# Kernel optimization log

Hardware: AMD Instinct MI355X
Metric: run time of the kernel (lower is better)

Reference implementation:

```python
import jax, jax.numpy as jnp
import numpy as np

GAMMA = 1.0
INPUT_DIM = 512
NUM_CENTERS = 4096
BATCH = 16384


def setup_inputs() -> dict:
    key = jax.random.key(0)
    kx, kc = jax.random.split(key)
    x = jax.random.normal(kx, (BATCH, INPUT_DIM), dtype=jnp.float32)
    centers = jax.random.normal(kc, (NUM_CENTERS, INPUT_DIM), dtype=jnp.float32)
    return {"x": x, "centers": centers}


def reference(x, centers):
    x_sq = jnp.sum(x * x, axis=-1, keepdims=True)            # [B, 1]
    c_sq = jnp.sum(centers * centers, axis=-1)               # [C]
    cross = jnp.einsum("bd,cd->bc", x, centers)              # [B, C]
    dist_sq = x_sq - 2.0 * cross + c_sq[None, :]
    return jnp.exp(-GAMMA * dist_sq)
```

## Files before the change

### kernel.cpp

```cpp
#include <hip/hip_runtime.h>
#include <stdint.h>

#define M_DIM 16384
#define N_DIM 4096
#define K_DIM 512

typedef int v8i __attribute__((ext_vector_type(8)));
typedef float f32x16 __attribute__((ext_vector_type(16)));
typedef float f32x4v __attribute__((ext_vector_type(4)));

typedef __attribute__((address_space(3))) uint32_t lds_u32_t;
typedef const __attribute__((address_space(1))) uint32_t glob_u32_t;

__device__ __forceinline__ void gload16(const void* g, void* l) {
    __builtin_amdgcn_global_load_lds((glob_u32_t*)g, (lds_u32_t*)l, 16, 0, 0);
}

__global__ __launch_bounds__(256)
void convert_norm_kernel(const float* __restrict__ X, const float* __restrict__ C,
                         uint8_t* __restrict__ Apack, uint8_t* __restrict__ Bf8,
                         float* __restrict__ xsq, float* __restrict__ csq) {
    const int wave = threadIdx.x >> 6;
    const int lane = threadIdx.x & 63;
    const int row = blockIdx.x * 4 + wave;

    const float* src;
    uint8_t* dst;
    float* nrm;
    int r;
    size_t off;
    if (row < M_DIM) {
        src = X; dst = Apack; nrm = xsq; r = row;
        off = (size_t)((r >> 5) * 8 + (lane >> 3)) * 2048
            + ((lane >> 2) & 1) * 1024 + (r & 31) * 32 + (lane & 3) * 8;
    } else {
        src = C; dst = Bf8; nrm = csq; r = row - M_DIM;
        off = (size_t)r * K_DIM + lane * 8;
    }

    const float4* p = (const float4*)(src + (size_t)r * K_DIM) + lane * 2;
    float4 a = p[0], b = p[1];
    uint32_t lo = 0, hi = 0;
    lo = __builtin_amdgcn_cvt_pk_fp8_f32(a.x, a.y, lo, false);
    lo = __builtin_amdgcn_cvt_pk_fp8_f32(a.z, a.w, lo, true);
    hi = __builtin_amdgcn_cvt_pk_fp8_f32(b.x, b.y, hi, false);
    hi = __builtin_amdgcn_cvt_pk_fp8_f32(b.z, b.w, hi, true);
    *(uint2*)(dst + off) = make_uint2(lo, hi);

    float s = a.x*a.x + a.y*a.y + a.z*a.z + a.w*a.w
            + b.x*b.x + b.y*b.y + b.z*b.z + b.w*b.w;
    #pragma unroll
    for (int o2 = 32; o2 > 0; o2 >>= 1) s += __shfl_down(s, o2, 64);
    if (lane == 0) nrm[r] = s;
}

__global__ __launch_bounds__(256, 4)
void rbf_mfma_kernel(const uint8_t* __restrict__ Apack, const uint8_t* __restrict__ B8,
                     const float* __restrict__ xsq, const float* __restrict__ csq,
                     float* __restrict__ out) {
    __shared__ uint8_t Bs[128 * 128];

    const int tid = threadIdx.x;
    const int lv  = tid & 63;
    const int w   = tid >> 6;
    const int h   = lv >> 5;
    const int r31 = lv & 31;

    const int bn = (blockIdx.x & 31) * 128;
    const int bm = (blockIdx.x >> 5) * 128;

    const int tr = tid >> 3;
    const int tc = tid & 7;
    const int cc = (tc - tr) & 7;
    const uint8_t* gB = B8 + (size_t)(bn + 4 * tr) * K_DIM + cc * 16;
    uint8_t* BsW = Bs + w * 1024;

    const uint8_t* aB = Apack + (size_t)((bm >> 5) + w) * 16384 + h * 1024 + r31 * 32;

    const uint8_t* bRow = Bs + r31 * 128;

    f32x16 acc[4] = {};

    for (int kk = 0; kk < 4; ++kk) {
        const int koff = kk * 128;
        #pragma unroll
        for (int R = 0; R < 4; ++R)
            gload16(gB + koff + (size_t)R * K_DIM, BsW + R * 4096);

        uint4 a0[2], a1[2];
        #pragma unroll
        for (int ksl = 0; ksl < 2; ++ksl) {
            const uint8_t* ap = aB + (2 * kk + ksl) * 2048;
            a0[ksl] = *(const uint4*)(ap);
            a1[ksl] = *(const uint4*)(ap + 16);
        }
        __syncthreads();

        #pragma unroll
        for (int ksl = 0; ksl < 2; ++ksl) {
            v8i av = (v8i){(int)a0[ksl].x, (int)a0[ksl].y, (int)a0[ksl].z, (int)a0[ksl].w,
                           (int)a1[ksl].x, (int)a1[ksl].y, (int)a1[ksl].z, (int)a1[ksl].w};
            const int c0 = ksl * 4 + 2 * h;
            const int s0 = ((c0 + 0 + r31) & 7) * 16;
            const int s1 = ((c0 + 1 + r31) & 7) * 16;
            #pragma unroll
            for (int j = 0; j < 4; ++j) {
                uint4 lo = *(const uint4*)(bRow + j * 4096 + s0);
                uint4 hi = *(const uint4*)(bRow + j * 4096 + s1);
                v8i bv = (v8i){(int)lo.x, (int)lo.y, (int)lo.z, (int)lo.w,
                               (int)hi.x, (int)hi.y, (int)hi.z, (int)hi.w};
                acc[j] = __builtin_amdgcn_mfma_scale_f32_32x32x64_f8f6f4(
                    av, bv, acc[j],
                    0 , 0 ,
                    0, 0x7F7F7F7Fu, 0, 0x7F7F7F7Fu);
            }
        }
        if (kk < 3) __syncthreads();
    }

    const float4 cs4 = *(const float4*)(csq + bn + 4 * r31);
    const int mbase = bm + 32 * w + 4 * h;

    #pragma unroll
    for (int g = 0; g < 4; ++g) {
        const float4 xs4 = *(const float4*)(xsq + mbase + 8 * g);
        #pragma unroll
        for (int rr = 0; rr < 4; ++rr) {
            const int reg = g * 4 + rr;
            const float xs = (rr == 0) ? xs4.x : (rr == 1) ? xs4.y
                           : (rr == 2) ? xs4.z : xs4.w;
            const int gm = mbase + 8 * g + rr;
            f32x4v o;
            o.x = __expf(-(xs - 2.0f * acc[0][reg] + cs4.x));
            o.y = __expf(-(xs - 2.0f * acc[1][reg] + cs4.y));
            o.z = __expf(-(xs - 2.0f * acc[2][reg] + cs4.z));
            o.w = __expf(-(xs - 2.0f * acc[3][reg] + cs4.w));
            __builtin_nontemporal_store(
                o, (f32x4v*)(out + (size_t)gm * N_DIM + bn + 4 * r31));
        }
    }
}

extern "C" void kernel_launch(void* const* d_in, const int* in_sizes, int n_in,
                              void* d_out, int out_size, void* d_ws, size_t ws_size,
                              hipStream_t stream) {
    const float* X = (const float*)d_in[0];
    const float* C = (const float*)d_in[1];
    float* out = (float*)d_out;

    uint8_t* Apack = (uint8_t*)d_ws;
    uint8_t* Bf8 = Apack + (size_t)M_DIM * K_DIM;
    float* xsq = (float*)(Bf8 + (size_t)N_DIM * K_DIM);
    float* csq = xsq + M_DIM;

    convert_norm_kernel<<<(M_DIM + N_DIM) / 4, 256, 0, stream>>>(X, C, Apack, Bf8, xsq, csq);
    rbf_mfma_kernel<<<(M_DIM / 128) * (N_DIM / 128), 256, 0, stream>>>(Apack, Bf8, xsq, csq, out);
}
```

Before: 301.1 us.

## Double K-chunk size for B tile and software-pipeline A fragment loads

Enlarges the shared B tile from 128 to 256 K-bytes per stage, so the K loop runs 2 iterations instead of 4 and needs half as many block barriers. The LDS swizzle changes to a 16-slot rotation, and the global-to-LDS copy mapping is rewritten to match. A fragments are now prefetched one K-slice ahead inside the inner loop rather than all loaded before the barrier. The cost is 32 KB of LDS per block instead of 16 KB, which may reduce occupancy.

```diff
diff --git a/kernel.cpp b/kernel.cpp
--- a/kernel.cpp
+++ b/kernel.cpp
@@ -58,7 +58,7 @@
 void rbf_mfma_kernel(const uint8_t* __restrict__ Apack, const uint8_t* __restrict__ B8,
                      const float* __restrict__ xsq, const float* __restrict__ csq,
                      float* __restrict__ out) {
-    __shared__ uint8_t Bs[128 * 128];
+    __shared__ uint8_t Bs[128 * 256];
 
     const int tid = threadIdx.x;
     const int lv  = tid & 63;
@@ -69,44 +69,46 @@
     const int bn = (blockIdx.x & 31) * 128;
     const int bm = (blockIdx.x >> 5) * 128;
 
-    const int tr = tid >> 3;
-    const int tc = tid & 7;
-    const int cc = (tc - tr) & 7;
-    const uint8_t* gB = B8 + (size_t)(bn + 4 * tr) * K_DIM + cc * 16;
+    const int q  = 4 * w + (lv >> 4);
+    const int s  = lv & 15;
+    const int cb = (s - q) & 15;
+    const uint8_t* gB0 = B8 + (size_t)(bn + 4 * q) * K_DIM + cb * 16;
     uint8_t* BsW = Bs + w * 1024;
 
     const uint8_t* aB = Apack + (size_t)((bm >> 5) + w) * 16384 + h * 1024 + r31 * 32;
 
-    const uint8_t* bRow = Bs + r31 * 128;
+    const uint8_t* bRow = Bs + r31 * 256;
 
     f32x16 acc[4] = {};
 
-    for (int kk = 0; kk < 4; ++kk) {
-        const int koff = kk * 128;
+    #pragma unroll
+    for (int kk = 0; kk < 2; ++kk) {
         #pragma unroll
-        for (int R = 0; R < 4; ++R)
-            gload16(gB + koff + (size_t)R * K_DIM, BsW + R * 4096);
-
-        uint4 a0[2], a1[2];
-        #pragma unroll
-        for (int ksl = 0; ksl < 2; ++ksl) {
-            const uint8_t* ap = aB + (2 * kk + ksl) * 2048;
-            a0[ksl] = *(const uint4*)(ap);
-            a1[ksl] = *(const uint4*)(ap + 16);
+        for (int R = 0; R < 8; ++R) {
+            const uint8_t* g = gB0 + (size_t)((R & 1) * 64) * K_DIM
+                             + (R >> 1) * K_DIM + kk * 256;
+            gload16(g, BsW + R * 4096);
         }
+        uint4 p0 = *(const uint4*)(aB + (4 * kk) * 2048);
+        uint4 p1 = *(const uint4*)(aB + (4 * kk) * 2048 + 16);
         __syncthreads();
 
         #pragma unroll
-        for (int ksl = 0; ksl < 2; ++ksl) {
-            v8i av = (v8i){(int)a0[ksl].x, (int)a0[ksl].y, (int)a0[ksl].z, (int)a0[ksl].w,
-                           (int)a1[ksl].x, (int)a1[ksl].y, (int)a1[ksl].z, (int)a1[ksl].w};
-            const int c0 = ksl * 4 + 2 * h;
-            const int s0 = ((c0 + 0 + r31) & 7) * 16;
-            const int s1 = ((c0 + 1 + r31) & 7) * 16;
+        for (int ksl = 0; ksl < 4; ++ksl) {
+            uint4 n0, n1;
+            if (ksl < 3) {
+                n0 = *(const uint4*)(aB + (4 * kk + ksl + 1) * 2048);
+                n1 = *(const uint4*)(aB + (4 * kk + ksl + 1) * 2048 + 16);
+            }
+            v8i av = (v8i){(int)p0.x, (int)p0.y, (int)p0.z, (int)p0.w,
+                           (int)p1.x, (int)p1.y, (int)p1.z, (int)p1.w};
+            const int c0 = 4 * ksl + 2 * h;
+            const int s0 = ((c0 + 0 + r31) & 15) * 16;
+            const int s1 = ((c0 + 1 + r31) & 15) * 16;
             #pragma unroll
             for (int j = 0; j < 4; ++j) {
-                uint4 lo = *(const uint4*)(bRow + j * 4096 + s0);
-                uint4 hi = *(const uint4*)(bRow + j * 4096 + s1);
+                uint4 lo = *(const uint4*)(bRow + j * 8192 + s0);
+                uint4 hi = *(const uint4*)(bRow + j * 8192 + s1);
                 v8i bv = (v8i){(int)lo.x, (int)lo.y, (int)lo.z, (int)lo.w,
                                (int)hi.x, (int)hi.y, (int)hi.z, (int)hi.w};
                 acc[j] = __builtin_amdgcn_mfma_scale_f32_32x32x64_f8f6f4(
@@ -114,8 +116,9 @@
                     0 , 0 ,
                     0, 0x7F7F7F7Fu, 0, 0x7F7F7F7Fu);
             }
+            p0 = n0; p1 = n1;
         }
-        if (kk < 3) __syncthreads();
+        if (kk == 0) __syncthreads();
     }
 
     const float4 cs4 = *(const float4*)(csq + bn + 4 * r31);
```

Result: slower. 319.9 us (+6.3%).
